# Optimization experiments

Measured on AMD Instinct MI355X. Metric: run time of the kernel, lower is better.

The kernel has to match this reference:

```python
import jax, jax.numpy as jnp
import numpy as np

B, N, D = 8, 4096, 128
P, K = 256, 64            # n_patches, n_pts_per_patch (= FoldingNet num_fine)
DFF, GRID = 1024, 2
G2 = GRID * GRID
NC = K // G2              # num_coarse
EPS = 1e-5                # BatchNorm eps (eval mode, running stats)


def fps(xyz, n):
    """Farthest point sampling on one cloud xyz [N,3] -> n int32 indices."""
    Np = xyz.shape[0]
    def step(carry, _):
        mind, last = carry
        d = jnp.sum((xyz - xyz[last]) ** 2, -1)
        mind = jnp.minimum(mind, d)
        nxt = jnp.argmax(mind).astype(jnp.int32)
        return (mind, nxt), nxt
    (_, _), idx = jax.lax.scan(step, (jnp.full((Np,), 1e10, xyz.dtype), jnp.int32(0)), None, length=n - 1)
    return jnp.concatenate([jnp.zeros((1,), jnp.int32), idx])


def setup_inputs() -> dict:
    key = jax.random.key(0)
    ks = jax.random.split(key, 24)
    rn = lambda i, s, sc=1.0: sc * jax.random.normal(ks[i], s, dtype=jnp.float32)
    inp = {
        'xyz': rn(0, (B, N, 3)),
        'feat': rn(1, (B, N, D)),
        # FoldingNet.xyz_mlp (Linear weights stored [in,out])
        'w1': rn(2, (D, DFF), 0.09), 'b1': rn(3, (DFF,), 0.02),
        'w2': rn(4, (DFF, DFF), 0.03), 'b2': rn(5, (DFF,), 0.02),
        'w3': rn(6, (DFF, 3 * NC), 0.03), 'b3': rn(7, (3 * NC,), 0.02),
        # FoldingNet.final_conv (1x1 conv weights stored [in,out]), BN eval stats
        'cw1': rn(8, (D + 5, DFF), 0.09), 'cb1': rn(9, (DFF,), 0.02),
        'g1': 0.5 + jax.random.uniform(ks[10], (DFF,), dtype=jnp.float32),
        'be1': rn(11, (DFF,), 0.02), 'm1': rn(12, (DFF,), 0.1),
        'v1': 0.5 + jax.random.uniform(ks[13], (DFF,), dtype=jnp.float32),
        'cw2': rn(14, (DFF, DFF), 0.03), 'cb2': rn(15, (DFF,), 0.02),
        'g2': 0.5 + jax.random.uniform(ks[16], (DFF,), dtype=jnp.float32),
        'be2': rn(17, (DFF,), 0.02), 'm2': rn(18, (DFF,), 0.1),
        'v2': 0.5 + jax.random.uniform(ks[19], (DFF,), dtype=jnp.float32),
        'cw3': rn(20, (DFF, 3), 0.03), 'cb3': rn(21, (3,), 0.02),
    }
    return inp


def reference(xyz, feat, w1, b1, w2, b2, w3, b3,
              cw1, cb1, g1, be1, m1, v1,
              cw2, cb2, g2, be2, m2, v2, cw3, cb3):
    # ---- point_forward: FPS -> square_distance -> masked topk -> gather -> maxpool ----
    fidx = jax.vmap(lambda p: fps(p, P))(xyz)                          # [B,P]
    patch_xyz = jnp.take_along_axis(xyz, fidx[:, :, None], 1)          # [B,P,3]
    d = (jnp.sum(xyz ** 2, -1)[:, :, None]
         + jnp.sum(patch_xyz ** 2, -1)[:, None, :]
         - 2.0 * jnp.einsum('bnc,bpc->bnp', xyz, patch_xyz))           # [B,N,P]
    # equal-sized dense batches => to_dense_batch mask is all-true (no 1e10 fill needed)
    _, gidx = jax.lax.top_k(-jnp.swapaxes(d, 1, 2), K)                 # [B,P,K] nearest
    bidx = jnp.arange(B)[:, None, None]
    grouped_feat = feat[bidx, gidx]                                    # [B,P,K,D]
    patch_feat = jnp.max(grouped_feat, axis=-2)                        # [B,P,D]
    grouped_xyz_norm = xyz[bidx, gidx] - patch_xyz[:, :, None, :]      # [B,P,K,3]

    # ---- FoldingNet decoder ----
    pf = patch_feat.reshape(B * P, D)
    h = jax.nn.relu(pf @ w1 + b1)
    h = jax.nn.relu(h @ w2 + b2)
    coarse = (h @ w3 + b3).reshape(B * P, NC, 3)                       # [BP,NC,3]
    pts = jnp.repeat(coarse, G2, axis=1)                               # [BP,K,3] (center)
    a = jnp.linspace(-0.05, 0.05, GRID, dtype=pf.dtype)
    seed2 = jnp.stack([jnp.tile(a, GRID), jnp.repeat(a, GRID)], -1)    # [G2,2]
    seedf = jnp.tile(seed2, (NC, 1))                                   # [K,2]
    featc = jnp.concatenate([
        jnp.broadcast_to(pf[:, None, :], (B * P, K, D)),
        jnp.broadcast_to(seedf[None], (B * P, K, 2)),
        pts], axis=-1)                                                 # [BP,K,D+5]
    bn = lambda x, g, be, m, v: (x - m) * (g * jax.lax.rsqrt(v + EPS)) + be
    h1 = jax.nn.relu(bn(featc @ cw1 + cb1, g1, be1, m1, v1))
    h2 = jax.nn.relu(bn(h1 @ cw2 + cb2, g2, be2, m2, v2))
    fine = h2 @ cw3 + cb3 + pts                                        # [BP,K,3]

    # ---- Chamfer L2 (mean(dist1)+mean(dist2)) between fine and grouped points ----
    gxyz = grouped_xyz_norm.reshape(B * P, K, 3)
    dd = jnp.sum((fine[:, :, None, :] - gxyz[:, None, :, :]) ** 2, -1) # [BP,K,K]
    loss_recon = jnp.mean(jnp.min(dd, axis=2)) + jnp.mean(jnp.min(dd, axis=1))
    return loss_recon
```

## Files before the change

### kernel.cpp

```cpp
#include <hip/hip_runtime.h>
#include <hip/hip_bf16.h>
#include <stdint.h>

#define DEV __device__ __forceinline__

using bf16x8  = __attribute__((ext_vector_type(8))) __bf16;
using floatx4 = __attribute__((ext_vector_type(4))) float;
using int32x8 = __attribute__((ext_vector_type(8))) int;

constexpr int Bb  = 8;
constexpr int Nn  = 4096;
constexpr int Dd  = 128;
constexpr int Pp  = 256;
constexpr int Kk  = 64;
constexpr int BP  = Bb * Pp;
constexpr int M2  = BP * Kk;
constexpr float EPSBN = 1e-5f;

DEV unsigned short f2bf(float f) {
  uint32_t u = __float_as_uint(f);
  u += 0x7fffu + ((u >> 16) & 1u);
  return (unsigned short)(u >> 16);
}
DEV float bf2f(unsigned short h) { return __uint_as_float(((uint32_t)h) << 16); }

DEV void async_copy16(const void* g, const void* l) {
  __builtin_amdgcn_global_load_lds(
      (__attribute__((address_space(1))) uint32_t*)(uintptr_t)g,
      (__attribute__((address_space(3))) uint32_t*)(uint32_t)(uintptr_t)l,
      16, 0, 0);
}

__global__ void prep_k(const float* g1, const float* be1, const float* m1, const float* v1, const float* cb1,
                       const float* g2, const float* be2, const float* m2, const float* v2, const float* cb2,
                       float* sc1, float* sh1, float* sc2, float* sh2, float* out) {
  int t = threadIdx.x;
  float s1 = g1[t] * rsqrtf(v1[t] + EPSBN);
  sc1[t] = s1; sh1[t] = (cb1[t] - m1[t]) * s1 + be1[t];
  float s2 = g2[t] * rsqrtf(v2[t] + EPSBN);
  sc2[t] = s2; sh2[t] = (cb2[t] - m2[t]) * s2 + be2[t];
  if (t == 0) out[0] = 0.f;
}

__global__ void cvt16(const float* __restrict__ in, unsigned short* __restrict__ out, int Kd, int Nd) {
  __shared__ float ts[32][33];
  int tx = threadIdx.x & 31, ty = threadIdx.x >> 5;
  int n0 = blockIdx.x * 32, k0 = blockIdx.y * 32;
#pragma unroll
  for (int r = 0; r < 4; ++r)
    ts[ty + 8 * r][tx] = in[(size_t)(k0 + ty + 8 * r) * Nd + n0 + tx];
  __syncthreads();
#pragma unroll
  for (int r = 0; r < 4; ++r)
    out[(size_t)(n0 + ty + 8 * r) * Kd + k0 + tx] = f2bf(ts[tx][ty + 8 * r]);
}

__global__ void cvt8(const float* __restrict__ in, uint8_t* __restrict__ out, int Kd, int Nd) {
  __shared__ float ts[32][33];
  int tx = threadIdx.x & 31, ty = threadIdx.x >> 5;
  int n0 = blockIdx.x * 32, k0 = blockIdx.y * 32;
#pragma unroll
  for (int r = 0; r < 4; ++r)
    ts[ty + 8 * r][tx] = in[(size_t)(k0 + ty + 8 * r) * Nd + n0 + tx];
  __syncthreads();
#pragma unroll
  for (int r = 0; r < 4; ++r) {
    float v = ts[tx][ty + 8 * r];
    int w = __builtin_amdgcn_cvt_pk_fp8_f32(v, v, 0, false);
    out[(size_t)(n0 + ty + 8 * r) * Kd + k0 + tx] = (uint8_t)(w & 0xff);
  }
}

#define DPPF(v, CTRL) __uint_as_float((uint32_t)__builtin_amdgcn_update_dpp( \
    (int)__float_as_uint(v), (int)__float_as_uint(v), CTRL, 0xF, 0xF, false))
#define DPPI(v, CTRL) __builtin_amdgcn_update_dpp(v, v, CTRL, 0xF, 0xF, false)
#define RSTEP2(CTRL) { \
    float od = DPPF(bv, CTRL); \
    int oi = DPPI(bi, CTRL); \
    bool tk = (od > bv) || (od == bv && oi < bi); \
    bv = tk ? od : bv; bi = tk ? oi : bi; }

__global__ __launch_bounds__(256)
void fps_k(const float* __restrict__ xyz, float* __restrict__ pxyz) {
  int b = blockIdx.x, tid = threadIdx.x;
  int lane = tid & 63, wv = tid >> 6;
  __shared__ float xs[Nn], ys[Nn], zs[Nn];
  __shared__ uint64_t cand[2][4];
  float xr[16], yr[16], zr[16], md[16];
#pragma unroll
  for (int j = 0; j < 16; ++j) {
    int i = tid + j * 256;
    const float* q = &xyz[(size_t)(b * Nn + i) * 3];
    float x = q[0], y = q[1], z = q[2];
    xr[j] = x; yr[j] = y; zr[j] = z; md[j] = 1e10f;
    xs[i] = x; ys[i] = y; zs[i] = z;
  }
  __syncthreads();
  const float* q0 = &xyz[(size_t)(b * Nn) * 3];
  float lx = q0[0], ly = q0[1], lz = q0[2];
  if (tid == 0) {
    pxyz[(size_t)(b * Pp) * 3 + 0] = lx;
    pxyz[(size_t)(b * Pp) * 3 + 1] = ly;
    pxyz[(size_t)(b * Pp) * 3 + 2] = lz;
  }
  for (int p = 1; p < Pp; ++p) {
    float bv = -1.f; int bi = 0x7fffffff;
#pragma unroll
    for (int j = 0; j < 16; ++j) {
      float dx = __fadd_rn(xr[j], -lx);
      float dy = __fadd_rn(yr[j], -ly);
      float dz = __fadd_rn(zr[j], -lz);
      float d = __fadd_rn(__fadd_rn(__fmul_rn(dx, dx), __fmul_rn(dy, dy)), __fmul_rn(dz, dz));
      float m = fminf(md[j], d);
      md[j] = m;
      if (m > bv) { bv = m; bi = tid + j * 256; }
    }
    RSTEP2(0x111) RSTEP2(0x112) RSTEP2(0x114) RSTEP2(0x118) RSTEP2(0x142) RSTEP2(0x143)
    int s = p & 1;
    if (lane == 63)
      cand[s][wv] = ((uint64_t)(uint32_t)__float_as_uint(bv) << 32) |
                    (uint32_t)(0x7fffffff - bi);
    __syncthreads();
    uint64_t k0 = cand[s][0], k1 = cand[s][1], k2 = cand[s][2], k3 = cand[s][3];
    uint64_t ka = (k0 > k1) ? k0 : k1;
    uint64_t kb = (k2 > k3) ? k2 : k3;
    uint64_t kw = (ka > kb) ? ka : kb;
    int wi = 0x7fffffff - (int)(uint32_t)(kw & 0xffffffffu);
    lx = xs[wi]; ly = ys[wi]; lz = zs[wi];
    if (tid == 0) {
      pxyz[(size_t)(b * Pp + p) * 3 + 0] = lx;
      pxyz[(size_t)(b * Pp + p) * 3 + 1] = ly;
      pxyz[(size_t)(b * Pp + p) * 3 + 2] = lz;
    }
  }
}

__global__ __launch_bounds__(256)
void group_k(const float* __restrict__ xyz, const float* __restrict__ feat,
             const float* __restrict__ pxyz, unsigned short* __restrict__ pfb,
             float* __restrict__ gxyz) {
  int bp = blockIdx.x, tid = threadIdx.x;
  int b = bp >> 8;
  __shared__ uint32_t dbits[Nn];
  __shared__ uint32_t hist[256];
  __shared__ int sel[64];
  __shared__ uint32_t svDigit, svWant, svClt, svCeq;
  __shared__ float red[256];
  float px = pxyz[(size_t)bp * 3], py = pxyz[(size_t)bp * 3 + 1], pz = pxyz[(size_t)bp * 3 + 2];
  for (int i = tid; i < Nn; i += 256) {
    const float* q = &xyz[(size_t)(b * Nn + i) * 3];
    float dx = q[0] - px, dy = q[1] - py, dz = q[2] - pz;
    dbits[i] = __float_as_uint(dx * dx + dy * dy + dz * dz);
  }
  uint32_t prefix = 0, want = 64;
  for (int shift = 24; shift >= 0; shift -= 8) {
    __syncthreads();
    hist[tid] = 0;
    __syncthreads();
    for (int i = tid; i < Nn; i += 256) {
      uint32_t v = dbits[i];
      bool match = (shift == 24) || ((v >> (shift + 8)) == prefix);
      if (match) atomicAdd(&hist[(v >> shift) & 255], 1u);
    }
    __syncthreads();
    uint32_t myh = hist[tid];
    for (int off = 1; off < 256; off <<= 1) {
      uint32_t o = (tid >= off) ? hist[tid - off] : 0u;
      __syncthreads();
      hist[tid] += o;
      __syncthreads();
    }
    uint32_t cum = hist[tid];
    uint32_t prev = cum - myh;
    if (prev < want && want <= cum) { svDigit = (uint32_t)tid; svWant = want - prev; }
    __syncthreads();
    prefix = (prefix << 8) | svDigit;
    want = svWant;
  }
  uint32_t tval = prefix;
  if (tid == 0) { svClt = 0; svCeq = 0; }
  __syncthreads();
  for (int i = tid; i < Nn; i += 256) {
    if (dbits[i] < tval) { uint32_t pos = atomicAdd(&svClt, 1u); sel[pos] = i; }
  }
  __syncthreads();
  uint32_t clt = svClt;
  for (int i = tid; i < Nn; i += 256) {
    if (dbits[i] == tval) {
      uint32_t pos = atomicAdd(&svCeq, 1u);
      if (clt + pos < 64) sel[clt + pos] = i;
    }
  }
  __syncthreads();
  if (tid < 192) {
    int k = tid / 3, c = tid - k * 3;
    float sub = (c == 0) ? px : (c == 1) ? py : pz;
    gxyz[(size_t)bp * 192 + tid] = xyz[(size_t)(b * Nn + sel[k]) * 3 + c] - sub;
  }
  int dch = tid & 127, half = tid >> 7;
  float m = -1e30f;
  for (int k = half * 32; k < half * 32 + 32; ++k)
    m = fmaxf(m, feat[(size_t)(b * Nn + sel[k]) * Dd + dch]);
  red[tid] = m;
  __syncthreads();
  if (half == 0) pfb[(size_t)bp * Dd + dch] = f2bf(fmaxf(m, red[tid + 128]));
}

template <int EPI>
__global__ __launch_bounds__(256)
void gemm_bt(const unsigned short* __restrict__ A, const unsigned short* __restrict__ Bt,
             float* __restrict__ Cf, unsigned short* __restrict__ Ch,
             const float* __restrict__ p0,
             int Npar, int Kd, int nbn) {
  __shared__ __align__(16) unsigned short As[128 * 32];
  __shared__ __align__(16) unsigned short Bs[128 * 32];
  const int tid = threadIdx.x;
  const int lane = tid & 63, wid = tid >> 6;
  const int bn = blockIdx.x % nbn, bm = blockIdx.x / nbn;
  const int m0 = bm * 128, n0 = bn * 128;
  const int quad = lane >> 4, l15 = lane & 15;
  const int wm = wid & 1, wn = wid >> 1;

  floatx4 acc[4][4];
#pragma unroll
  for (int i = 0; i < 4; ++i)
#pragma unroll
    for (int j = 0; j < 4; ++j) acc[i][j] = floatx4{0.f, 0.f, 0.f, 0.f};

  const int c0i = tid, c1i = tid + 256;
  const int r0 = c0i >> 2, o0 = (c0i & 3) * 8;
  const int r1 = c1i >> 2, o1 = (c1i & 3) * 8;

  for (int k0 = 0; k0 < Kd; k0 += 32) {
    async_copy16(A + (size_t)(m0 + r0) * Kd + k0 + o0, &As[c0i * 8]);
    async_copy16(A + (size_t)(m0 + r1) * Kd + k0 + o1, &As[c1i * 8]);
    async_copy16(Bt + (size_t)(n0 + r0) * Kd + k0 + o0, &Bs[c0i * 8]);
    async_copy16(Bt + (size_t)(n0 + r1) * Kd + k0 + o1, &Bs[c1i * 8]);
    __syncthreads();
    const bf16x8* Ap = reinterpret_cast<const bf16x8*>(As);
    const bf16x8* Bp = reinterpret_cast<const bf16x8*>(Bs);
    bf16x8 af[4], bfv[4];
#pragma unroll
    for (int t = 0; t < 4; ++t) {
      af[t]  = Ap[(wm * 64 + t * 16 + l15) * 4 + quad];
      bfv[t] = Bp[(wn * 64 + t * 16 + l15) * 4 + quad];
    }
#pragma unroll
    for (int mt = 0; mt < 4; ++mt)
#pragma unroll
      for (int nt = 0; nt < 4; ++nt)
        acc[mt][nt] = __builtin_amdgcn_mfma_f32_16x16x32_bf16(af[mt], bfv[nt], acc[mt][nt], 0, 0, 0);
    __syncthreads();
  }

  const int rowBase = m0 + wm * 64 + quad * 4;
  const int colBase = n0 + wn * 64 + l15;

  if (EPI == 0) {
#pragma unroll
    for (int mt = 0; mt < 4; ++mt)
#pragma unroll
      for (int nt = 0; nt < 4; ++nt)
#pragma unroll
        for (int r = 0; r < 4; ++r)
          Cf[(size_t)(rowBase + mt * 16 + r) * Npar + colBase + nt * 16] = acc[mt][nt][r];
  } else {
#pragma unroll
    for (int nt = 0; nt < 4; ++nt) {
      float bias = p0[colBase + nt * 16];
#pragma unroll
      for (int mt = 0; mt < 4; ++mt)
#pragma unroll
        for (int r = 0; r < 4; ++r) {
          float v = fmaxf(acc[mt][nt][r] + bias, 0.f);
          Ch[(size_t)(rowBase + mt * 16 + r) * Npar + colBase + nt * 16] = f2bf(v);
        }
    }
  }
}

__global__ __launch_bounds__(256)
void gemm_mx3(const uint8_t* __restrict__ A, const uint8_t* __restrict__ Bt,
              const float* __restrict__ p0, const float* __restrict__ p1,
              const float* __restrict__ cw3, float* __restrict__ partial,
              int rowOff, int nbm, int Kd) {
  __shared__ __align__(128) uint8_t As[128 * 128];
  __shared__ __align__(128) uint8_t Bs[128 * 128];
  const int tid = threadIdx.x;
  const int lane = tid & 63, wid = tid >> 6;
  const int bm = blockIdx.x % nbm, bn = blockIdx.x / nbm;
  const int m0 = bm * 128, n0 = bn * 128;
  const int quad = lane >> 4, l15 = lane & 15;
  const int wm = wid & 1, wn = wid >> 1;

  floatx4 acc[4][4];
#pragma unroll
  for (int i = 0; i < 4; ++i)
#pragma unroll
    for (int j = 0; j < 4; ++j) acc[i][j] = floatx4{0.f, 0.f, 0.f, 0.f};

  for (int k0 = 0; k0 < Kd; k0 += 128) {
#pragma unroll
    for (int c = 0; c < 4; ++c) {
      int ci = c * 256 + tid;
      int row = ci >> 3, cp = ci & 7;
      int cc = cp ^ (row & 7);
      async_copy16(A + (size_t)(m0 + row) * Kd + k0 + cc * 16, &As[ci * 16]);
      async_copy16(Bt + (size_t)(n0 + row) * Kd + k0 + cc * 16, &Bs[ci * 16]);
    }
    __syncthreads();
    const uint4* Ap = (const uint4*)As;
    const uint4* Bp = (const uint4*)Bs;
    int32x8 av[4], bv[4];
#pragma unroll
    for (int t = 0; t < 4; ++t) {
      int rm = wm * 64 + t * 16 + l15;
      int rn = wn * 64 + t * 16 + l15;
      int swm = rm & 7, swn = rn & 7;
      uint4 alo = Ap[rm * 8 + ((2 * quad) ^ swm)];
      uint4 ahi = Ap[rm * 8 + ((2 * quad + 1) ^ swm)];
      uint4 blo = Bp[rn * 8 + ((2 * quad) ^ swn)];
      uint4 bhi = Bp[rn * 8 + ((2 * quad + 1) ^ swn)];
      av[t] = int32x8{(int)alo.x, (int)alo.y, (int)alo.z, (int)alo.w,
                      (int)ahi.x, (int)ahi.y, (int)ahi.z, (int)ahi.w};
      bv[t] = int32x8{(int)blo.x, (int)blo.y, (int)blo.z, (int)blo.w,
                      (int)bhi.x, (int)bhi.y, (int)bhi.z, (int)bhi.w};
    }
#pragma unroll
    for (int mt = 0; mt < 4; ++mt)
#pragma unroll
      for (int nt = 0; nt < 4; ++nt)
        acc[mt][nt] = __builtin_amdgcn_mfma_scale_f32_16x16x128_f8f6f4(
            av[mt], bv[nt], acc[mt][nt], 0, 0, 0, 127, 0, 127);
    __syncthreads();
  }

  const int rowBase = m0 + wm * 64 + quad * 4;
  const int colBase = n0 + wn * 64 + l15;
  float fp[4][4][3];
#pragma unroll
  for (int mt = 0; mt < 4; ++mt)
#pragma unroll
    for (int r = 0; r < 4; ++r)
      fp[mt][r][0] = fp[mt][r][1] = fp[mt][r][2] = 0.f;
#pragma unroll
  for (int nt = 0; nt < 4; ++nt) {
    int col = colBase + nt * 16;
    float sc = p0[col], sh = p1[col];
    float c0 = cw3[col * 3], c1 = cw3[col * 3 + 1], c2 = cw3[col * 3 + 2];
#pragma unroll
    for (int mt = 0; mt < 4; ++mt)
#pragma unroll
      for (int r = 0; r < 4; ++r) {
        float v = fmaxf(acc[mt][nt][r] * sc + sh, 0.f);
        fp[mt][r][0] += v * c0; fp[mt][r][1] += v * c1; fp[mt][r][2] += v * c2;
      }
  }
#pragma unroll
  for (int off = 1; off < 16; off <<= 1)
#pragma unroll
    for (int mt = 0; mt < 4; ++mt)
#pragma unroll
      for (int r = 0; r < 4; ++r)
#pragma unroll
        for (int i = 0; i < 3; ++i)
          fp[mt][r][i] += __shfl_xor(fp[mt][r][i], off, 64);
  if (l15 == 0) {
    int slice = bn * 2 + wn;
#pragma unroll
    for (int mt = 0; mt < 4; ++mt)
#pragma unroll
      for (int r = 0; r < 4; ++r) {
        int row = rowOff + rowBase + mt * 16 + r;
#pragma unroll
        for (int i = 0; i < 3; ++i)
          partial[((size_t)slice * M2 + row) * 3 + i] = fp[mt][r][i];
      }
  }
}

__global__ void finered_k(const float* __restrict__ partial, const float* __restrict__ coarse,
                          const float* __restrict__ cb3, float* __restrict__ fine) {
  int t = blockIdx.x * 256 + threadIdx.x;
  if (t >= M2 * 3) return;
  int i = t % 3;
  int r = t / 3;
  int bp = r >> 6, k = r & 63, j = k >> 2;
  float s = cb3[i] + coarse[(size_t)bp * 48 + j * 3 + i];
#pragma unroll
  for (int sl = 0; sl < 16; ++sl) s += partial[((size_t)sl * M2 + r) * 3 + i];
  fine[t] = s;
}

__global__ __launch_bounds__(256)
void coarse_k(const unsigned short* __restrict__ h2m, const float* __restrict__ w3,
              const float* __restrict__ b3, float* __restrict__ coarse) {
  int r = blockIdx.x, tid = threadIdx.x;
  __shared__ float hrow[1024];
  __shared__ float part[192];
  for (int i = tid; i < 1024; i += 256) hrow[i] = bf2f(h2m[(size_t)r * 1024 + i]);
  __syncthreads();
  if (tid < 192) {
    int j = tid % 48, seg = tid / 48;
    float acc = 0.f;
    for (int k = seg * 256; k < seg * 256 + 256; ++k) acc += hrow[k] * w3[(size_t)k * 48 + j];
    part[tid] = acc;
  }
  __syncthreads();
  if (tid < 48)
    coarse[(size_t)r * 48 + tid] = part[tid] + part[tid + 48] + part[tid + 96] + part[tid + 144] + b3[tid];
}

__global__ __launch_bounds__(256)
void h1build_k(const float* __restrict__ u1, const float* __restrict__ cw1,
               const float* __restrict__ coarse, const float* __restrict__ sc1,
               const float* __restrict__ sh1, uint8_t* __restrict__ h1) {
  int bp = blockIdx.x, tid = threadIdx.x;
  __shared__ float co[48];
  if (tid < 48) co[tid] = coarse[(size_t)bp * 48 + tid];
  __syncthreads();
  int n0 = tid * 4;
  float4 un  = *(const float4*)&u1[(size_t)bp * 1024 + n0];
  float4 a0  = *(const float4*)&cw1[128 * 1024 + n0];
  float4 a1  = *(const float4*)&cw1[129 * 1024 + n0];
  float4 b0  = *(const float4*)&cw1[130 * 1024 + n0];
  float4 b1v = *(const float4*)&cw1[131 * 1024 + n0];
  float4 b2v = *(const float4*)&cw1[132 * 1024 + n0];
  float4 sc  = *(const float4*)&sc1[n0];
  float4 sh  = *(const float4*)&sh1[n0];
  const float sxv[4] = {-0.05f, 0.05f, -0.05f, 0.05f};
  const float syv[4] = {-0.05f, -0.05f, 0.05f, 0.05f};
  float s[4][4];
#pragma unroll
  for (int g = 0; g < 4; ++g) {
    s[g][0] = sxv[g] * a0.x + syv[g] * a1.x;
    s[g][1] = sxv[g] * a0.y + syv[g] * a1.y;
    s[g][2] = sxv[g] * a0.z + syv[g] * a1.z;
    s[g][3] = sxv[g] * a0.w + syv[g] * a1.w;
  }
  uint32_t* out = (uint32_t*)h1;
  for (int k = 0; k < 64; ++k) {
    int j = k >> 2, g = k & 3;
    float c0 = co[j * 3], c1 = co[j * 3 + 1], c2 = co[j * 3 + 2];
    float x0 = un.x + s[g][0] + c0 * b0.x + c1 * b1v.x + c2 * b2v.x;
    float x1 = un.y + s[g][1] + c0 * b0.y + c1 * b1v.y + c2 * b2v.y;
    float x2 = un.z + s[g][2] + c0 * b0.z + c1 * b1v.z + c2 * b2v.z;
    float x3 = un.w + s[g][3] + c0 * b0.w + c1 * b1v.w + c2 * b2v.w;
    float v0 = fmaxf(x0 * sc.x + sh.x, 0.f);
    float v1 = fmaxf(x1 * sc.y + sh.y, 0.f);
    float v2 = fmaxf(x2 * sc.z + sh.z, 0.f);
    float v3 = fmaxf(x3 * sc.w + sh.w, 0.f);
    int w = __builtin_amdgcn_cvt_pk_fp8_f32(v0, v1, 0, false);
    w = __builtin_amdgcn_cvt_pk_fp8_f32(v2, v3, w, true);
    out[(size_t)(bp * 64 + k) * 256 + tid] = (uint32_t)w;
  }
}

__global__ __launch_bounds__(256)
void chamfer_k(const float* __restrict__ fine, const float* __restrict__ gxyz,
               float* __restrict__ out) {
  int tid = threadIdx.x, wv = tid >> 6, lane = tid & 63;
  int bp = blockIdx.x * 4 + wv;
  __shared__ float sf[4][64][3], sg[4][64][3];
  const float* fr = &fine[(size_t)(bp * 64 + lane) * 3];
  const float* gr = &gxyz[(size_t)(bp * 64 + lane) * 3];
  sf[wv][lane][0] = fr[0]; sf[wv][lane][1] = fr[1]; sf[wv][lane][2] = fr[2];
  sg[wv][lane][0] = gr[0]; sg[wv][lane][1] = gr[1]; sg[wv][lane][2] = gr[2];
  __syncthreads();
  float f0 = sf[wv][lane][0], f1 = sf[wv][lane][1], f2 = sf[wv][lane][2];
  float g0 = sg[wv][lane][0], g1 = sg[wv][lane][1], g2 = sg[wv][lane][2];
  float rmin = 1e30f, cmin = 1e30f;
  for (int j = 0; j < 64; ++j) {
    float dx = f0 - sg[wv][j][0], dy = f1 - sg[wv][j][1], dz = f2 - sg[wv][j][2];
    rmin = fminf(rmin, dx * dx + dy * dy + dz * dz);
    float ex = sf[wv][j][0] - g0, ey = sf[wv][j][1] - g1, ez = sf[wv][j][2] - g2;
    cmin = fminf(cmin, ex * ex + ey * ey + ez * ez);
  }
  float tot = rmin + cmin;
  for (int off = 32; off; off >>= 1) tot += __shfl_down(tot, off, 64);
  if (lane == 0) atomicAdd(out, tot * (1.0f / 131072.0f));
}

extern "C" void kernel_launch(void* const* d_in, const int* in_sizes, int n_in,
                              void* d_out, int out_size, void* d_ws, size_t ws_size,
                              hipStream_t stream) {
  (void)in_sizes; (void)n_in; (void)out_size;
  const float* xyz = (const float*)d_in[0];
  const float* feat = (const float*)d_in[1];
  const float* w1 = (const float*)d_in[2];
  const float* b1 = (const float*)d_in[3];
  const float* w2 = (const float*)d_in[4];
  const float* b2 = (const float*)d_in[5];
  const float* w3 = (const float*)d_in[6];
  const float* b3 = (const float*)d_in[7];
  const float* cw1 = (const float*)d_in[8];
  const float* cb1 = (const float*)d_in[9];
  const float* g1 = (const float*)d_in[10];
  const float* be1 = (const float*)d_in[11];
  const float* m1 = (const float*)d_in[12];
  const float* v1 = (const float*)d_in[13];
  const float* cw2 = (const float*)d_in[14];
  const float* cb2 = (const float*)d_in[15];
  const float* g2 = (const float*)d_in[16];
  const float* be2 = (const float*)d_in[17];
  const float* m2 = (const float*)d_in[18];
  const float* v2 = (const float*)d_in[19];
  const float* cw3 = (const float*)d_in[20];
  const float* cb3 = (const float*)d_in[21];
  float* out = (float*)d_out;

  uint8_t* ws = (uint8_t*)d_ws;
  size_t off = 0;
  auto alloc = [&](size_t bytes) {
    void* p = ws + off;
    off = (off + bytes + 255) & ~(size_t)255;
    return p;
  };
  float*          pxyz  = (float*)alloc((size_t)BP * 3 * 4);
  unsigned short* w1t   = (unsigned short*)alloc((size_t)1024 * 128 * 2);
  unsigned short* cw1t  = (unsigned short*)alloc((size_t)1024 * 128 * 2);
  unsigned short* w2t   = (unsigned short*)alloc((size_t)1024 * 1024 * 2);
  uint8_t*        cw2t8 = (uint8_t*)alloc((size_t)1024 * 1024);
  float*          sc1   = (float*)alloc(4096);
  float*          sh1   = (float*)alloc(4096);
  float*          sc2   = (float*)alloc(4096);
  float*          sh2   = (float*)alloc(4096);
  unsigned short* pfb   = (unsigned short*)alloc((size_t)BP * 128 * 2);
  float*          gxyz  = (float*)alloc((size_t)BP * 64 * 3 * 4);
  float*          u1    = (float*)alloc((size_t)BP * 1024 * 4);
  unsigned short* hb    = (unsigned short*)alloc((size_t)BP * 1024 * 2);
  unsigned short* h2m   = (unsigned short*)alloc((size_t)BP * 1024 * 2);
  float*          coarse = (float*)alloc((size_t)BP * 48 * 4);
  float*          fine  = (float*)alloc((size_t)M2 * 3 * 4);
  float*          partial = (float*)alloc((size_t)16 * M2 * 3 * 4);

  size_t perPatch = (size_t)Kk * 1024;
  size_t avail = (ws_size > off) ? (ws_size - off - 256) : 0;
  int ppc = 2;
  while (ppc < BP && (size_t)(ppc * 2) * perPatch <= avail) ppc *= 2;
  uint8_t* h1 = (uint8_t*)alloc((size_t)ppc * perPatch);
  int nch = BP / ppc;

  prep_k<<<1, 1024, 0, stream>>>(g1, be1, m1, v1, cb1, g2, be2, m2, v2, cb2,
                                 sc1, sh1, sc2, sh2, out);
  cvt16<<<dim3(1024 / 32, 128 / 32), 256, 0, stream>>>(w1, w1t, 128, 1024);
  cvt16<<<dim3(1024 / 32, 128 / 32), 256, 0, stream>>>(cw1, cw1t, 128, 1024);
  cvt16<<<dim3(1024 / 32, 1024 / 32), 256, 0, stream>>>(w2, w2t, 1024, 1024);
  cvt8<<<dim3(1024 / 32, 1024 / 32), 256, 0, stream>>>(cw2, cw2t8, 1024, 1024);
  fps_k<<<Bb, 256, 0, stream>>>(xyz, pxyz);
  group_k<<<BP, 256, 0, stream>>>(xyz, feat, pxyz, pfb, gxyz);
  gemm_bt<0><<<(2048 / 128) * 8, 256, 0, stream>>>(pfb, cw1t, u1, nullptr, nullptr,
                                                   1024, 128, 8);
  gemm_bt<1><<<(2048 / 128) * 8, 256, 0, stream>>>(pfb, w1t, nullptr, hb, b1,
                                                   1024, 128, 8);
  gemm_bt<1><<<(2048 / 128) * 8, 256, 0, stream>>>(hb, w2t, nullptr, h2m, b2,
                                                   1024, 1024, 8);
  coarse_k<<<2048, 256, 0, stream>>>(h2m, w3, b3, coarse);
  for (int c = 0; c < nch; ++c) {
    int pstart = c * ppc;
    int nbm = ppc * Kk / 128;
    h1build_k<<<ppc, 256, 0, stream>>>(u1 + (size_t)pstart * 1024, cw1,
                                       coarse + (size_t)pstart * 48, sc1, sh1, h1);
    gemm_mx3<<<nbm * 8, 256, 0, stream>>>(
        h1, cw2t8, sc2, sh2, cw3, partial, pstart * Kk, nbm, 1024);
  }
  finered_k<<<(M2 * 3 + 255) / 256, 256, 0, stream>>>(partial, coarse, cb3, fine);
  chamfer_k<<<BP / 4, 256, 0, stream>>>(fine, gxyz, out);
}
```

Measured before the change: 703.4 us.

## Fuse fine-point reduction into FP8 GEMM by looping all N-tiles per block

```diff
diff --git a/kernel.cpp b/kernel.cpp
--- a/kernel.cpp
+++ b/kernel.cpp
@@ -282,80 +282,86 @@
 __global__ __launch_bounds__(256)
 void gemm_mx3(const uint8_t* __restrict__ A, const uint8_t* __restrict__ Bt,
               const float* __restrict__ p0, const float* __restrict__ p1,
-              const float* __restrict__ cw3, float* __restrict__ partial,
-              int rowOff, int nbm, int Kd) {
+              const float* __restrict__ cw3, const float* __restrict__ coarse,
+              const float* __restrict__ cb3, float* __restrict__ fine,
+              int rowOff, int Kd) {
   __shared__ __align__(128) uint8_t As[128 * 128];
   __shared__ __align__(128) uint8_t Bs[128 * 128];
+  __shared__ float fsum[2][2][64][3];
   const int tid = threadIdx.x;
   const int lane = tid & 63, wid = tid >> 6;
-  const int bm = blockIdx.x % nbm, bn = blockIdx.x / nbm;
-  const int m0 = bm * 128, n0 = bn * 128;
+  const int bm = blockIdx.x;
+  const int m0 = bm * 128;
   const int quad = lane >> 4, l15 = lane & 15;
   const int wm = wid & 1, wn = wid >> 1;
 
-  floatx4 acc[4][4];
-#pragma unroll
-  for (int i = 0; i < 4; ++i)
-#pragma unroll
-    for (int j = 0; j < 4; ++j) acc[i][j] = floatx4{0.f, 0.f, 0.f, 0.f};
-
-  for (int k0 = 0; k0 < Kd; k0 += 128) {
-#pragma unroll
-    for (int c = 0; c < 4; ++c) {
-      int ci = c * 256 + tid;
-      int row = ci >> 3, cp = ci & 7;
-      int cc = cp ^ (row & 7);
-      async_copy16(A + (size_t)(m0 + row) * Kd + k0 + cc * 16, &As[ci * 16]);
-      async_copy16(Bt + (size_t)(n0 + row) * Kd + k0 + cc * 16, &Bs[ci * 16]);
-    }
-    __syncthreads();
-    const uint4* Ap = (const uint4*)As;
-    const uint4* Bp = (const uint4*)Bs;
-    int32x8 av[4], bv[4];
-#pragma unroll
-    for (int t = 0; t < 4; ++t) {
-      int rm = wm * 64 + t * 16 + l15;
-      int rn = wn * 64 + t * 16 + l15;
-      int swm = rm & 7, swn = rn & 7;
-      uint4 alo = Ap[rm * 8 + ((2 * quad) ^ swm)];
-      uint4 ahi = Ap[rm * 8 + ((2 * quad + 1) ^ swm)];
-      uint4 blo = Bp[rn * 8 + ((2 * quad) ^ swn)];
-      uint4 bhi = Bp[rn * 8 + ((2 * quad + 1) ^ swn)];
-      av[t] = int32x8{(int)alo.x, (int)alo.y, (int)alo.z, (int)alo.w,
-                      (int)ahi.x, (int)ahi.y, (int)ahi.z, (int)ahi.w};
-      bv[t] = int32x8{(int)blo.x, (int)blo.y, (int)blo.z, (int)blo.w,
-                      (int)bhi.x, (int)bhi.y, (int)bhi.z, (int)bhi.w};
-    }
-#pragma unroll
-    for (int mt = 0; mt < 4; ++mt)
-#pragma unroll
-      for (int nt = 0; nt < 4; ++nt)
-        acc[mt][nt] = __builtin_amdgcn_mfma_scale_f32_16x16x128_f8f6f4(
-            av[mt], bv[nt], acc[mt][nt], 0, 0, 0, 127, 0, 127);
-    __syncthreads();
-  }
-
-  const int rowBase = m0 + wm * 64 + quad * 4;
-  const int colBase = n0 + wn * 64 + l15;
   float fp[4][4][3];
 #pragma unroll
   for (int mt = 0; mt < 4; ++mt)
 #pragma unroll
     for (int r = 0; r < 4; ++r)
       fp[mt][r][0] = fp[mt][r][1] = fp[mt][r][2] = 0.f;
-#pragma unroll
-  for (int nt = 0; nt < 4; ++nt) {
-    int col = colBase + nt * 16;
-    float sc = p0[col], sh = p1[col];
-    float c0 = cw3[col * 3], c1 = cw3[col * 3 + 1], c2 = cw3[col * 3 + 2];
-#pragma unroll
-    for (int mt = 0; mt < 4; ++mt)
-#pragma unroll
-      for (int r = 0; r < 4; ++r) {
-        float v = fmaxf(acc[mt][nt][r] * sc + sh, 0.f);
-        fp[mt][r][0] += v * c0; fp[mt][r][1] += v * c1; fp[mt][r][2] += v * c2;
+
+  for (int bn = 0; bn < 8; ++bn) {
+    const int n0 = bn * 128;
+    floatx4 acc[4][4];
+#pragma unroll
+    for (int i = 0; i < 4; ++i)
+#pragma unroll
+      for (int j = 0; j < 4; ++j) acc[i][j] = floatx4{0.f, 0.f, 0.f, 0.f};
+
+    for (int k0 = 0; k0 < Kd; k0 += 128) {
+#pragma unroll
+      for (int c = 0; c < 4; ++c) {
+        int ci = c * 256 + tid;
+        int row = ci >> 3, cp = ci & 7;
+        int cc = cp ^ (row & 7);
+        async_copy16(A + (size_t)(m0 + row) * Kd + k0 + cc * 16, &As[ci * 16]);
+        async_copy16(Bt + (size_t)(n0 + row) * Kd + k0 + cc * 16, &Bs[ci * 16]);
       }
-  }
+      __syncthreads();
+      const uint4* Ap = (const uint4*)As;
+      const uint4* Bp = (const uint4*)Bs;
+      int32x8 av[4], bv[4];
+#pragma unroll
+      for (int t = 0; t < 4; ++t) {
+        int rm = wm * 64 + t * 16 + l15;
+        int rn = wn * 64 + t * 16 + l15;
+        int swm = rm & 7, swn = rn & 7;
+        uint4 alo = Ap[rm * 8 + ((2 * quad) ^ swm)];
+        uint4 ahi = Ap[rm * 8 + ((2 * quad + 1) ^ swm)];
+        uint4 blo = Bp[rn * 8 + ((2 * quad) ^ swn)];
+        uint4 bhi = Bp[rn * 8 + ((2 * quad + 1) ^ swn)];
+        av[t] = int32x8{(int)alo.x, (int)alo.y, (int)alo.z, (int)alo.w,
+                        (int)ahi.x, (int)ahi.y, (int)ahi.z, (int)ahi.w};
+        bv[t] = int32x8{(int)blo.x, (int)blo.y, (int)blo.z, (int)blo.w,
+                        (int)bhi.x, (int)bhi.y, (int)bhi.z, (int)bhi.w};
+      }
+#pragma unroll
+      for (int mt = 0; mt < 4; ++mt)
+#pragma unroll
+        for (int nt = 0; nt < 4; ++nt)
+          acc[mt][nt] = __builtin_amdgcn_mfma_scale_f32_16x16x128_f8f6f4(
+              av[mt], bv[nt], acc[mt][nt], 0, 0, 0, 127, 0, 127);
+      __syncthreads();
+    }
+
+    const int colBase = n0 + wn * 64 + l15;
+#pragma unroll
+    for (int nt = 0; nt < 4; ++nt) {
+      int col = colBase + nt * 16;
+      float sc = p0[col], sh = p1[col];
+      float c0 = cw3[col * 3], c1 = cw3[col * 3 + 1], c2 = cw3[col * 3 + 2];
+#pragma unroll
+      for (int mt = 0; mt < 4; ++mt)
+#pragma unroll
+        for (int r = 0; r < 4; ++r) {
+          float v = fmaxf(acc[mt][nt][r] * sc + sh, 0.f);
+          fp[mt][r][0] += v * c0; fp[mt][r][1] += v * c1; fp[mt][r][2] += v * c2;
+        }
+    }
+  }
+
 #pragma unroll
   for (int off = 1; off < 16; off <<= 1)
 #pragma unroll
@@ -366,30 +372,23 @@
         for (int i = 0; i < 3; ++i)
           fp[mt][r][i] += __shfl_xor(fp[mt][r][i], off, 64);
   if (l15 == 0) {
-    int slice = bn * 2 + wn;
 #pragma unroll
     for (int mt = 0; mt < 4; ++mt)
 #pragma unroll
       for (int r = 0; r < 4; ++r) {
-        int row = rowOff + rowBase + mt * 16 + r;
-#pragma unroll
-        for (int i = 0; i < 3; ++i)
-          partial[((size_t)slice * M2 + row) * 3 + i] = fp[mt][r][i];
+        int rowLocal = quad * 4 + mt * 16 + r;
+#pragma unroll
+        for (int i = 0; i < 3; ++i) fsum[wm][wn][rowLocal][i] = fp[mt][r][i];
       }
   }
-}
-
-__global__ void finered_k(const float* __restrict__ partial, const float* __restrict__ coarse,
-                          const float* __restrict__ cb3, float* __restrict__ fine) {
-  int t = blockIdx.x * 256 + threadIdx.x;
-  if (t >= M2 * 3) return;
-  int i = t % 3;
-  int r = t / 3;
-  int bp = r >> 6, k = r & 63, j = k >> 2;
-  float s = cb3[i] + coarse[(size_t)bp * 48 + j * 3 + i];
-#pragma unroll
-  for (int sl = 0; sl < 16; ++sl) s += partial[((size_t)sl * M2 + r) * 3 + i];
-  fine[t] = s;
+  __syncthreads();
+  for (int t = tid; t < 128 * 3; t += 256) {
+    int row = t / 3, i = t - row * 3;
+    float s = fsum[row >> 6][0][row & 63][i] + fsum[row >> 6][1][row & 63][i];
+    int g = rowOff + m0 + row;
+    int bp = g >> 6, kp = g & 63, j = kp >> 2;
+    fine[(size_t)g * 3 + i] = s + cb3[i] + coarse[(size_t)bp * 48 + j * 3 + i];
+  }
 }
 
 __global__ __launch_bounds__(256)
@@ -532,7 +531,6 @@
   unsigned short* h2m   = (unsigned short*)alloc((size_t)BP * 1024 * 2);
   float*          coarse = (float*)alloc((size_t)BP * 48 * 4);
   float*          fine  = (float*)alloc((size_t)M2 * 3 * 4);
-  float*          partial = (float*)alloc((size_t)16 * M2 * 3 * 4);
 
   size_t perPatch = (size_t)Kk * 1024;
   size_t avail = (ws_size > off) ? (ws_size - off - 256) : 0;
@@ -561,9 +559,8 @@
     int nbm = ppc * Kk / 128;
     h1build_k<<<ppc, 256, 0, stream>>>(u1 + (size_t)pstart * 1024, cw1,
                                        coarse + (size_t)pstart * 48, sc1, sh1, h1);
-    gemm_mx3<<<nbm * 8, 256, 0, stream>>>(
-        h1, cw2t8, sc2, sh2, cw3, partial, pstart * Kk, nbm, 1024);
-  }
-  finered_k<<<(M2 * 3 + 255) / 256, 256, 0, stream>>>(partial, coarse, cb3, fine);
+    gemm_mx3<<<nbm, 256, 0, stream>>>(
+        h1, cw2t8, sc2, sh2, cw3, coarse, cb3, fine, pstart * Kk, 1024);
+  }
   chamfer_k<<<BP / 4, 256, 0, stream>>>(fine, gxyz, out);
 }
```

Measured after the change: 645.9 us. 8.2% less time.
